# Kernel optimization log

Measured on AMD Instinct MI355X. Metric: run time of the kernel, lower is better.

The kernel has to match this reference:

```python
import jax, jax.numpy as jnp
import numpy as np

B, S, K = 32, 16384, 64  # batch, num_samples, num_clusters


def _neg_idx(num_clusters):
    # Static column indices kept per row by mask_correlated_samples: drop
    # the diagonal and the (i, K+i)/(K+i, i) positive pairs -> N-2 cols/row.
    N = 2 * num_clusters
    idx = []
    for r in range(N):
        partner = r + num_clusters if r < num_clusters else r - num_clusters
        idx.append([c for c in range(N) if c != r and c != partner])
    return np.asarray(idx, dtype=np.int32)  # [N, N-2]


def target_distribution(q):
    # q: [S, K]. weight = q^2 / colsum; then row-normalize.
    w = q ** 2.0 / jnp.sum(q, axis=0)
    return w / jnp.sum(w, axis=1, keepdims=True)


def setup_inputs() -> dict:
    key = jax.random.key(0)
    k1, k2 = jax.random.split(key)
    q_i = jax.random.uniform(k1, (B, S, K), dtype=jnp.float32)
    q_j = jax.random.uniform(k2, (B, S, K), dtype=jnp.float32)
    temperature_l = jnp.asarray(1.0, dtype=jnp.float32)
    return {"q_i": q_i, "q_j": q_j, "temperature_l": temperature_l}


def reference(q_i, q_j, temperature_l):
    num_clusters = q_i.shape[2]
    N = 2 * num_clusters
    neg_idx = jnp.asarray(_neg_idx(num_clusters))  # static, [N, N-2]
    rows = jnp.arange(N)[:, None]

    def per_batch(qi_b, qj_b):
        pi = target_distribution(qi_b).T  # [K, S]
        pj = target_distribution(qj_b).T  # [K, S]
        q = jnp.concatenate([pi, pj], axis=0)        # [N, S]
        sim = jnp.matmul(q, q.T) / temperature_l      # [N, N]
        pos = jnp.concatenate(
            [jnp.diagonal(sim, num_clusters), jnp.diagonal(sim, -num_clusters)]
        )[:, None]                                    # [N, 1]
        neg = sim[rows, neg_idx]                      # [N, N-2]
        logits = jnp.concatenate([pos, neg], axis=1)  # [N, N-1], label = 0
        # CrossEntropyLoss(reduction='sum') with labels all zero
        loss = jnp.sum(jax.nn.logsumexp(logits, axis=1) - logits[:, 0])
        return loss / N

    losses = jax.vmap(per_batch)(q_i, q_j)  # [B]
    return jnp.mean(losses)
```

## Files before the change

### kernel.cpp

```cpp
#include <hip/hip_runtime.h>
#include <math.h>

#define Bn 32
#define Sn 16384
#define Kn 64
#define Nn 128

#define P1  8
#define NSB 32
#define SPB (Sn/NSB)
#define NCH (SPB/32)

typedef __attribute__((ext_vector_type(8))) short bf16x8;
typedef __attribute__((ext_vector_type(4))) float f32x4;

#define WS_CSPART 0
#define WS_CS     (Bn*2*P1*64)
#define WS_GRAM   (WS_CS + Bn*2*64)
#define WS_LOSS   (WS_GRAM + Bn*3*4096)
#define WS_PART   (WS_LOSS + Bn)
#define WS_PART_SZ ((size_t)Bn*NSB*3*4096)

__device__ __forceinline__ unsigned short f2bf(float f) {
    unsigned int u = __float_as_uint(f);
    u += 0x7FFFu + ((u >> 16) & 1u);
    return (unsigned short)(u >> 16);
}

__global__ __launch_bounds__(256) void k_colsum(const float* __restrict__ qi,
                                                const float* __restrict__ qj,
                                                float* __restrict__ ws) {
    const int blk   = blockIdx.x;
    const int chunk = blk % P1;
    const int pair  = blk / P1;
    const int v = pair & 1, b = pair >> 1;
    const float* __restrict__ src = v ? qj : qi;
    const int tid = threadIdx.x;
    const int c4 = (tid & 15) * 4;
    const int sg = tid >> 4;
    const long base = (long)b * Sn * Kn + (long)chunk * (Sn / P1) * Kn;

    float4 acc = make_float4(0.f, 0.f, 0.f, 0.f);
    for (int s = sg; s < Sn / P1; s += 16) {
        const float4 q = *(const float4*)(src + base + (long)s * Kn + c4);
        acc.x += q.x; acc.y += q.y; acc.z += q.z; acc.w += q.w;
    }
    __shared__ float red[16 * 64];
    *(float4*)&red[sg * 64 + c4] = acc;
    __syncthreads();
    if (tid < 64) {
        float s = 0.f;
        #pragma unroll
        for (int g = 0; g < 16; ++g) s += red[g * 64 + tid];
        ws[WS_CSPART + (pair * P1 + chunk) * 64 + tid] = s;
    }
}

__global__ void k_colsum_reduce(float* __restrict__ ws) {
    const int pair = blockIdx.x;
    const int tid = threadIdx.x;
    float s = 0.f;
    #pragma unroll
    for (int p = 0; p < P1; ++p) s += ws[WS_CSPART + (pair * P1 + p) * 64 + tid];
    ws[WS_CS + pair * 64 + tid] = s;
}

template<int ATOMIC>
__global__ __launch_bounds__(256, 4) void k_gram(const float* __restrict__ qi,
                                                 const float* __restrict__ qj,
                                                 float* __restrict__ ws) {
    const int b   = blockIdx.x / NSB;
    const int sb  = blockIdx.x % NSB;
    const int tid = threadIdx.x;
    const int w   = tid >> 6;
    const int l   = tid & 63;
    const int lc  = tid & 15;
    const int sp  = tid >> 4;
    const int c0  = lc * 4;

    __shared__ unsigned short lp[2][64 * 40];

    const float4 csI = *(const float4*)&ws[WS_CS + (b * 2 + 0) * 64 + c0];
    const float4 csJ = *(const float4*)&ws[WS_CS + (b * 2 + 1) * 64 + c0];
    const float icI[4] = {1.f / csI.x, 1.f / csI.y, 1.f / csI.z, 1.f / csI.w};
    const float icJ[4] = {1.f / csJ.x, 1.f / csJ.y, 1.f / csJ.z, 1.f / csJ.w};

    f32x4 aII[4], aIJ[4], aJJ[4];
    #pragma unroll
    for (int t = 0; t < 4; ++t) {
        aII[t] = (f32x4){0.f, 0.f, 0.f, 0.f};
        aIJ[t] = (f32x4){0.f, 0.f, 0.f, 0.f};
        aJJ[t] = (f32x4){0.f, 0.f, 0.f, 0.f};
    }

    const long bb  = (long)b * Sn * Kn;
    const long s0g = (long)sb * SPB;

    for (int ct = 0; ct < NCH; ++ct) {
        #pragma unroll
        for (int v = 0; v < 2; ++v) {
            const float* __restrict__ src = v ? qj : qi;
            const float* ic = v ? icJ : icI;
            const long off = bb + (s0g + ct * 32 + 2 * sp) * (long)Kn + c0;
            const float4 qa = *(const float4*)(src + off);
            const float4 qb = *(const float4*)(src + off + Kn);
            float wa[4] = {qa.x * qa.x * ic[0], qa.y * qa.y * ic[1],
                           qa.z * qa.z * ic[2], qa.w * qa.w * ic[3]};
            float wb[4] = {qb.x * qb.x * ic[0], qb.y * qb.y * ic[1],
                           qb.z * qb.z * ic[2], qb.w * qb.w * ic[3]};
            float ra = wa[0] + wa[1] + wa[2] + wa[3];
            float rb = wb[0] + wb[1] + wb[2] + wb[3];
            #pragma unroll
            for (int d = 1; d < 16; d <<= 1) {
                ra += __shfl_xor(ra, d);
                rb += __shfl_xor(rb, d);
            }
            const float ia = 1.f / ra, ib = 1.f / rb;
            #pragma unroll
            for (int cc = 0; cc < 4; ++cc) {
                const unsigned int pk = (unsigned int)f2bf(wa[cc] * ia)
                                      | ((unsigned int)f2bf(wb[cc] * ib) << 16);
                *(unsigned int*)&lp[v][(c0 + cc) * 40 + 2 * sp] = pk;
            }
        }
        __syncthreads();

        const int sgo = (l >> 4) * 8;
        bf16x8 fi[4], fj[4];
        #pragma unroll
        for (int t = 0; t < 4; ++t) {
            fi[t] = *(const bf16x8*)&lp[0][(t * 16 + lc) * 40 + sgo];
            fj[t] = *(const bf16x8*)&lp[1][(t * 16 + lc) * 40 + sgo];
        }
        const bf16x8 ai = *(const bf16x8*)&lp[0][(w * 16 + lc) * 40 + sgo];
        const bf16x8 aj = *(const bf16x8*)&lp[1][(w * 16 + lc) * 40 + sgo];
        #pragma unroll
        for (int nt = 0; nt < 4; ++nt) {
            aII[nt] = __builtin_amdgcn_mfma_f32_16x16x32_bf16(ai, fi[nt], aII[nt], 0, 0, 0);
            aIJ[nt] = __builtin_amdgcn_mfma_f32_16x16x32_bf16(ai, fj[nt], aIJ[nt], 0, 0, 0);
            aJJ[nt] = __builtin_amdgcn_mfma_f32_16x16x32_bf16(aj, fj[nt], aJJ[nt], 0, 0, 0);
        }
        __syncthreads();
    }

    const int row0 = w * 16 + (l >> 4) * 4;
    if (ATOMIC) {
        float* __restrict__ dst = ws + WS_GRAM + (long)b * 3 * 4096;
        #pragma unroll
        for (int nt = 0; nt < 4; ++nt) {
            #pragma unroll
            for (int r = 0; r < 4; ++r) {
                const int e = (row0 + r) * 64 + nt * 16 + lc;
                atomicAdd(&dst[e],        aII[nt][r]);
                atomicAdd(&dst[4096 + e], aIJ[nt][r]);
                atomicAdd(&dst[8192 + e], aJJ[nt][r]);
            }
        }
    } else {
        float* __restrict__ dst = ws + WS_PART + (long)(b * NSB + sb) * 3 * 4096;
        #pragma unroll
        for (int nt = 0; nt < 4; ++nt) {
            #pragma unroll
            for (int r = 0; r < 4; ++r) {
                const int e = (row0 + r) * 64 + nt * 16 + lc;
                dst[e]        = aII[nt][r];
                dst[4096 + e] = aIJ[nt][r];
                dst[8192 + e] = aJJ[nt][r];
            }
        }
    }
}

__global__ __launch_bounds__(256) void k_gram_reduce(float* __restrict__ ws) {
    const int idx = blockIdx.x * 256 + threadIdx.x;
    const int b = idx / (3 * 4096);
    const int e = idx % (3 * 4096);
    float s = 0.f;
    #pragma unroll 8
    for (int p = 0; p < NSB; ++p)
        s += ws[WS_PART + (long)(b * NSB + p) * 3 * 4096 + e];
    ws[WS_GRAM + (long)b * 3 * 4096 + e] = s;
}

__device__ __forceinline__ float sim_entry(const float* __restrict__ g, int r, int c) {
    if (r < 64) return (c < 64) ? g[r * 64 + c] : g[4096 + r * 64 + (c - 64)];
    return (c < 64) ? g[4096 + c * 64 + (r - 64)] : g[8192 + (r - 64) * 64 + (c - 64)];
}

__global__ __launch_bounds__(128) void k_loss(const float* __restrict__ temp,
                                              float* __restrict__ ws) {
    const int b = blockIdx.x;
    const int r = threadIdx.x;
    const float* __restrict__ g = ws + WS_GRAM + (long)b * 3 * 4096;
    const float inv_t = 1.f / temp[0];
    const int p = r ^ 64;

    float m = -1e30f, pos = 0.f;
    for (int c = 0; c < Nn; ++c) {
        if (c == r) continue;
        const float v = sim_entry(g, r, c) * inv_t;
        m = fmaxf(m, v);
        if (c == p) pos = v;
    }
    float sum = 0.f;
    for (int c = 0; c < Nn; ++c) {
        if (c == r) continue;
        const float v = sim_entry(g, r, c) * inv_t;
        sum += expf(v - m);
    }
    const float val = m + logf(sum) - pos;

    __shared__ float red[Nn];
    red[r] = val;
    __syncthreads();
    for (int st = 64; st > 0; st >>= 1) {
        if (r < st) red[r] += red[r + st];
        __syncthreads();
    }
    if (r == 0) ws[WS_LOSS + b] = red[0] / (float)Nn;
}

__global__ void k_final(float* __restrict__ ws, float* __restrict__ out) {
    if (threadIdx.x == 0) {
        float s = 0.f;
        for (int b = 0; b < Bn; ++b) s += ws[WS_LOSS + b];
        out[0] = s / (float)Bn;
    }
}

extern "C" void kernel_launch(void* const* d_in, const int* in_sizes, int n_in,
                              void* d_out, int out_size, void* d_ws, size_t ws_size,
                              hipStream_t stream) {
    const float* qi   = (const float*)d_in[0];
    const float* qj   = (const float*)d_in[1];
    const float* temp = (const float*)d_in[2];
    float* ws  = (float*)d_ws;
    float* out = (float*)d_out;

    const size_t need_f = (size_t)WS_PART + WS_PART_SZ;
    const bool partial = ws_size >= need_f * sizeof(float);

    k_colsum<<<Bn * 2 * P1, 256, 0, stream>>>(qi, qj, ws);
    k_colsum_reduce<<<Bn * 2, 64, 0, stream>>>(ws);

    if (partial) {
        k_gram<0><<<Bn * NSB, 256, 0, stream>>>(qi, qj, ws);
        k_gram_reduce<<<(Bn * 3 * 4096) / 256, 256, 0, stream>>>(ws);
    } else {
        hipMemsetAsync(ws + WS_GRAM, 0, (size_t)Bn * 3 * 4096 * sizeof(float), stream);
        k_gram<1><<<Bn * NSB, 256, 0, stream>>>(qi, qj, ws);
    }

    k_loss<<<Bn, 128, 0, stream>>>(temp, ws);
    k_final<<<1, 64, 0, stream>>>(ws, out);
}
```

Measured before the change: 190.2 us.

## Double-buffer gram LDS tiles with register prefetch; widen colsum grid and unroll

Result: faster. 166.1 us (-12.7%).

```diff
diff --git a/kernel.cpp b/kernel.cpp
--- a/kernel.cpp
+++ b/kernel.cpp
@@ -6,7 +6,7 @@
 #define Kn 64
 #define Nn 128
 
-#define P1  8
+#define P1  32
 #define NSB 32
 #define SPB (Sn/NSB)
 #define NCH (SPB/32)
@@ -39,10 +39,12 @@
     const int c4 = (tid & 15) * 4;
     const int sg = tid >> 4;
     const long base = (long)b * Sn * Kn + (long)chunk * (Sn / P1) * Kn;
+    const float* __restrict__ p0 = src + base + (long)sg * Kn + c4;
 
     float4 acc = make_float4(0.f, 0.f, 0.f, 0.f);
-    for (int s = sg; s < Sn / P1; s += 16) {
-        const float4 q = *(const float4*)(src + base + (long)s * Kn + c4);
+    #pragma unroll 8
+    for (int s = 0; s < (Sn / P1) / 16; ++s) {
+        const float4 q = *(const float4*)(p0 + (long)s * 16 * Kn);
         acc.x += q.x; acc.y += q.y; acc.z += q.z; acc.w += q.w;
     }
     __shared__ float red[16 * 64];
@@ -78,7 +80,7 @@
     const int sp  = tid >> 4;
     const int c0  = lc * 4;
 
-    __shared__ unsigned short lp[2][64 * 40];
+    __shared__ unsigned short lp[2][2][64 * 40];
 
     const float4 csI = *(const float4*)&ws[WS_CS + (b * 2 + 0) * 64 + c0];
     const float4 csJ = *(const float4*)&ws[WS_CS + (b * 2 + 1) * 64 + c0];
@@ -96,14 +98,20 @@
     const long bb  = (long)b * Sn * Kn;
     const long s0g = (long)sb * SPB;
 
-    for (int ct = 0; ct < NCH; ++ct) {
+    float4 pfa[2], pfb[2];
+
+    auto issue = [&](int ct) {
+        const long off = bb + (s0g + ct * 32 + 2 * sp) * (long)Kn + c0;
+        pfa[0] = *(const float4*)(qi + off);
+        pfb[0] = *(const float4*)(qi + off + Kn);
+        pfa[1] = *(const float4*)(qj + off);
+        pfb[1] = *(const float4*)(qj + off + Kn);
+    };
+    auto stage = [&](int buf) {
         #pragma unroll
         for (int v = 0; v < 2; ++v) {
-            const float* __restrict__ src = v ? qj : qi;
             const float* ic = v ? icJ : icI;
-            const long off = bb + (s0g + ct * 32 + 2 * sp) * (long)Kn + c0;
-            const float4 qa = *(const float4*)(src + off);
-            const float4 qb = *(const float4*)(src + off + Kn);
+            const float4 qa = pfa[v], qb = pfb[v];
             float wa[4] = {qa.x * qa.x * ic[0], qa.y * qa.y * ic[1],
                            qa.z * qa.z * ic[2], qa.w * qa.w * ic[3]};
             float wb[4] = {qb.x * qb.x * ic[0], qb.y * qb.y * ic[1],
@@ -120,25 +128,32 @@
             for (int cc = 0; cc < 4; ++cc) {
                 const unsigned int pk = (unsigned int)f2bf(wa[cc] * ia)
                                       | ((unsigned int)f2bf(wb[cc] * ib) << 16);
-                *(unsigned int*)&lp[v][(c0 + cc) * 40 + 2 * sp] = pk;
-            }
-        }
-        __syncthreads();
-
-        const int sgo = (l >> 4) * 8;
-        bf16x8 fi[4], fj[4];
-        #pragma unroll
-        for (int t = 0; t < 4; ++t) {
-            fi[t] = *(const bf16x8*)&lp[0][(t * 16 + lc) * 40 + sgo];
-            fj[t] = *(const bf16x8*)&lp[1][(t * 16 + lc) * 40 + sgo];
-        }
-        const bf16x8 ai = *(const bf16x8*)&lp[0][(w * 16 + lc) * 40 + sgo];
-        const bf16x8 aj = *(const bf16x8*)&lp[1][(w * 16 + lc) * 40 + sgo];
+                *(unsigned int*)&lp[buf][v][(c0 + cc) * 40 + 2 * sp] = pk;
+            }
+        }
+    };
+
+    issue(0);
+    stage(0);
+    issue(1);
+    __syncthreads();
+
+    const int sgo = (l >> 4) * 8;
+    for (int ct = 0; ct < NCH; ++ct) {
+        const int cur = ct & 1;
+        const bf16x8 ai = *(const bf16x8*)&lp[cur][0][(w * 16 + lc) * 40 + sgo];
+        const bf16x8 aj = *(const bf16x8*)&lp[cur][1][(w * 16 + lc) * 40 + sgo];
         #pragma unroll
         for (int nt = 0; nt < 4; ++nt) {
-            aII[nt] = __builtin_amdgcn_mfma_f32_16x16x32_bf16(ai, fi[nt], aII[nt], 0, 0, 0);
-            aIJ[nt] = __builtin_amdgcn_mfma_f32_16x16x32_bf16(ai, fj[nt], aIJ[nt], 0, 0, 0);
-            aJJ[nt] = __builtin_amdgcn_mfma_f32_16x16x32_bf16(aj, fj[nt], aJJ[nt], 0, 0, 0);
+            const bf16x8 fi = *(const bf16x8*)&lp[cur][0][(nt * 16 + lc) * 40 + sgo];
+            const bf16x8 fj = *(const bf16x8*)&lp[cur][1][(nt * 16 + lc) * 40 + sgo];
+            aII[nt] = __builtin_amdgcn_mfma_f32_16x16x32_bf16(ai, fi, aII[nt], 0, 0, 0);
+            aIJ[nt] = __builtin_amdgcn_mfma_f32_16x16x32_bf16(ai, fj, aIJ[nt], 0, 0, 0);
+            aJJ[nt] = __builtin_amdgcn_mfma_f32_16x16x32_bf16(aj, fj, aJJ[nt], 0, 0, 0);
+        }
+        if (ct + 1 < NCH) {
+            stage(cur ^ 1);
+            if (ct + 2 < NCH) issue(ct + 2);
         }
         __syncthreads();
     }
```
